# Performance work log

Hardware: AMD Instinct MI355X
Metric: run time of the kernel (lower is better)

## Reference

```python
import jax, jax.numpy as jnp
import numpy as np

B, L, D, H, DH, DL, NB = 8, 1024, 512, 8, 64, 64, 128
EPS = 1e-6


def layer_norm(x, g, b):
    m = jnp.mean(x, axis=-1, keepdims=True)
    v = jnp.mean((x - m) ** 2, axis=-1, keepdims=True)
    return (x - m) * jax.lax.rsqrt(v + EPS) * g + b


def rel_bias(timestamps, pos_w, ts_w):
    # position part: skew trick, pos_w has length 2L-1
    t = jnp.concatenate([pos_w, jnp.zeros((L,), pos_w.dtype)])  # (3L-1,)
    t = jnp.tile(t, L)[:-L].reshape(L, 3 * L - 2)
    rel_pos = t[:, L - 1:2 * L - 1]  # (L, L)
    # timestamp part: bucketized pairwise diffs of extended timestamps
    ext = jnp.concatenate([timestamps, timestamps[:, L - 1:L]], axis=1)  # (B, L+1)
    d = ext[:, 1:, None] - ext[:, None, :-1]  # (B, L, L)
    mag = jnp.maximum(jnp.abs(d).astype(jnp.float32), 1.0)
    bucket = jnp.clip((jnp.log(mag) / 0.301).astype(jnp.int32), 0, NB)
    rel_ts = ts_w[bucket]  # (B, L, L)
    return rel_pos[None] + rel_ts


def setup_inputs() -> dict:
    key = jax.random.key(0)
    ks = jax.random.split(key, 8)
    x = jax.random.normal(ks[0], (B, L, D), dtype=jnp.float32)
    timestamps = jnp.sort(jax.random.randint(ks[1], (B, L), 0, 1000000, dtype=jnp.int64), axis=1)
    attn_mask = jnp.triu(jnp.ones((L, L), jnp.float32), k=1)[None, None]  # 1 = masked (future)
    total_out = 2 * DL * H + 2 * DH * H
    uvqk_w = jax.random.normal(ks[2], (D, total_out), dtype=jnp.float32) * 0.02
    out_w = jax.random.normal(ks[3], (DL * H, D), dtype=jnp.float32) * 0.02
    out_b = jnp.zeros((D,), jnp.float32)
    ln1_g = jnp.ones((D,), jnp.float32); ln1_b = jnp.zeros((D,), jnp.float32)
    ln2_g = jnp.ones((DL * H,), jnp.float32); ln2_b = jnp.zeros((DL * H,), jnp.float32)
    ts_weights = jax.random.normal(ks[4], (NB + 1,), dtype=jnp.float32) * 0.02
    pos_weights = jax.random.normal(ks[5], (2 * L - 1,), dtype=jnp.float32) * 0.02
    return {"x": x, "timestamps": timestamps, "attn_mask": attn_mask,
            "uvqk_w": uvqk_w, "out_w": out_w, "out_b": out_b,
            "ln1_g": ln1_g, "ln1_b": ln1_b, "ln2_g": ln2_g, "ln2_b": ln2_b,
            "ts_weights": ts_weights, "pos_weights": pos_weights}


def reference(x, timestamps, attn_mask, uvqk_w, out_w, out_b,
              ln1_g, ln1_b, ln2_g, ln2_b, ts_weights, pos_weights):
    z = layer_norm(x, ln1_g, ln1_b)
    z = jax.nn.silu(z @ uvqk_w)  # linear_activation == 'silu'
    u, v, q, k = jnp.split(z, [DL * H, 2 * DL * H, 2 * DL * H + DH * H], axis=-1)
    q = q.reshape(B, L, H, DH)
    k = k.reshape(B, L, H, DH)
    v = v.reshape(B, L, H, DL)
    scores = jnp.einsum('bmhd,bnhd->bhmn', q, k)
    scores = scores + rel_bias(timestamps, pos_weights, ts_weights)[:, None]
    scores = jax.nn.silu(scores) / L * (1.0 - attn_mask)
    z = jnp.einsum('bhmn,bnhd->bmhd', scores, v).reshape(B, L, H * DL)
    z = layer_norm(z, ln2_g, ln2_b) * u  # gated LN
    return z @ out_w + out_b + x
```

## Files before the change

kernel.cpp:

```cpp
#include <hip/hip_runtime.h>
#include <math.h>

constexpr int Bc = 8;
constexpr int Lc = 1024;
constexpr int Dc = 512;
constexpr int Hc = 8;
constexpr int DHc = 64;
constexpr int DLc = 64;
constexpr int NBc = 128;
constexpr int TOTAL_OUT = 2 * DLc * Hc + 2 * DHc * Hc;
constexpr int ROWS = Bc * Lc;

using f32x4 = __attribute__((ext_vector_type(4))) float;
using s16x8 = __attribute__((ext_vector_type(8))) short;

__device__ __forceinline__ float bf2f(ushort u) {
    union { unsigned int i; float f; } v; v.i = ((unsigned int)u) << 16; return v.f;
}
__device__ __forceinline__ ushort f2bf(float f) {
    union { float f; unsigned int i; } v; v.f = f;
    unsigned int r = v.i + 0x7fffu + ((v.i >> 16) & 1u);
    return (ushort)(r >> 16);
}
__device__ __forceinline__ float silu(float x) {
    float e = __expf(-x);
    return x * __builtin_amdgcn_rcpf(1.0f + e);
}

__global__ __launch_bounds__(256) void transpose_cast(const float* __restrict__ in,
                                                      ushort* __restrict__ out,
                                                      int R, int C) {
    __shared__ float tile[32][33];
    int bc = blockIdx.x * 32, br = blockIdx.y * 32;
    int tx = threadIdx.x & 31, ty = threadIdx.x >> 5;
    for (int i = ty; i < 32; i += 8) {
        int r = br + i, c = bc + tx;
        tile[i][tx] = (r < R && c < C) ? in[(size_t)r * C + c] : 0.f;
    }
    __syncthreads();
    for (int i = ty; i < 32; i += 8) {
        int c = bc + i, r = br + tx;
        if (c < C && r < R) out[(size_t)c * R + r] = f2bf(tile[tx][i]);
    }
}

__global__ __launch_bounds__(256) void ln1_kernel(const float* __restrict__ x,
                                                  const float* __restrict__ g,
                                                  const float* __restrict__ bta,
                                                  ushort* __restrict__ outp) {
    int wid = threadIdx.x >> 6, lane = threadIdx.x & 63;
    int row = blockIdx.x * 4 + wid;
    const float4* xr = (const float4*)(x + (size_t)row * Dc);
    float4 a = xr[lane * 2], c = xr[lane * 2 + 1];
    float xv[8] = {a.x, a.y, a.z, a.w, c.x, c.y, c.z, c.w};
    float s = 0.f, q = 0.f;
#pragma unroll
    for (int i = 0; i < 8; i++) { s += xv[i]; q += xv[i] * xv[i]; }
#pragma unroll
    for (int off = 32; off; off >>= 1) { s += __shfl_xor(s, off); q += __shfl_xor(q, off); }
    float mean = s * (1.f / 512.f);
    float var  = q * (1.f / 512.f) - mean * mean;
    float rstd = rsqrtf(var + 1e-6f);
    const float4* gv = (const float4*)g; const float4* bv = (const float4*)bta;
    float4 g0 = gv[lane * 2], g1 = gv[lane * 2 + 1];
    float4 b0 = bv[lane * 2], b1 = bv[lane * 2 + 1];
    float G[8] = {g0.x, g0.y, g0.z, g0.w, g1.x, g1.y, g1.z, g1.w};
    float Bv[8] = {b0.x, b0.y, b0.z, b0.w, b1.x, b1.y, b1.z, b1.w};
    union { ushort u16[8]; uint4 v; } pk;
#pragma unroll
    for (int i = 0; i < 8; i++) pk.u16[i] = f2bf((xv[i] - mean) * rstd * G[i] + Bv[i]);
    ((uint4*)(outp + (size_t)row * Dc))[lane] = pk.v;
}

__global__ __launch_bounds__(256) void bias_kernel(const int* __restrict__ ts,
                                                   const float* __restrict__ pos_w,
                                                   const float* __restrict__ ts_w,
                                                   ushort* __restrict__ biasb) {
    __shared__ float posw[2 * Lc - 1];
    __shared__ float tsw[NBc + 1];
    int tid = threadIdx.x;
    int b = blockIdx.y;
    for (int i = tid; i < 2 * Lc - 1; i += 256) posw[i] = pos_w[i];
    if (tid < NBc + 1) tsw[tid] = ts_w[tid];
    __syncthreads();
    int m = blockIdx.x * 8 + (tid >> 5);
    int n0 = (tid & 31) * 32;
    const int* tsb = ts + b * Lc;
    int mp = m + 1 < Lc ? m + 1 : Lc - 1;
    int tsm = tsb[mp];
    int pbase = (Lc - 1) + n0 - m;
    union { ushort u16[32]; uint4 v[4]; } o;
#pragma unroll
    for (int i = 0; i < 32; i += 4) {
        int4 tn = *(const int4*)&tsb[n0 + i];
        int dv[4] = {tsm - tn.x, tsm - tn.y, tsm - tn.z, tsm - tn.w};
#pragma unroll
        for (int e = 0; e < 4; e++) {
            float mag = fmaxf(fabsf((float)dv[e]), 1.f);
            int bkt = (int)(__log2f(mag) * 2.3028147f);
            bkt = bkt < 0 ? 0 : (bkt > NBc ? NBc : bkt);
            o.u16[i + e] = f2bf(posw[pbase + i + e] + tsw[bkt]);
        }
    }
    uint4* dst = (uint4*)&biasb[((size_t)b * Lc + m) * Lc + n0];
#pragma unroll
    for (int i = 0; i < 4; i++) dst[i] = o.v[i];
}

__global__ __launch_bounds__(256) void gemm1_kernel(const ushort* __restrict__ A,
                                                    const ushort* __restrict__ Bt,
                                                    ushort* __restrict__ Ub,
                                                    ushort* __restrict__ VTg,
                                                    ushort* __restrict__ Qb,
                                                    ushort* __restrict__ Kb) {
    __shared__ __align__(16) ushort As[128][72];
    __shared__ __align__(16) ushort Bs[128][72];
    int tid = threadIdx.x;
    int m0 = blockIdx.x * 128, n0 = blockIdx.y * 128;
    int w = tid >> 6, lane = tid & 63;
    int wm = (w >> 1) * 64, wn = (w & 1) * 64;
    f32x4 acc[4][4] = {};
    for (int k0 = 0; k0 < Dc; k0 += 64) {
        __syncthreads();
#pragma unroll
        for (int c = tid; c < 1024; c += 256) {
            int r = c >> 3, c8 = c & 7;
            *(uint4*)&As[r][c8 * 8] = *(const uint4*)&A[(size_t)(m0 + r) * Dc + k0 + c8 * 8];
            *(uint4*)&Bs[r][c8 * 8] = *(const uint4*)&Bt[(size_t)(n0 + r) * Dc + k0 + c8 * 8];
        }
        __syncthreads();
#pragma unroll
        for (int ks = 0; ks < 2; ++ks) {
            int kb = ks * 32 + (lane >> 4) * 8;
            s16x8 af[4], bfr[4];
#pragma unroll
            for (int i = 0; i < 4; i++) af[i] = *(const s16x8*)&As[wm + i * 16 + (lane & 15)][kb];
#pragma unroll
            for (int j = 0; j < 4; j++) bfr[j] = *(const s16x8*)&Bs[wn + j * 16 + (lane & 15)][kb];
#pragma unroll
            for (int i = 0; i < 4; i++)
#pragma unroll
                for (int j = 0; j < 4; j++)
                    acc[i][j] = __builtin_amdgcn_mfma_f32_16x16x32_bf16(af[i], bfr[j], acc[i][j], 0, 0, 0);
        }
    }
    int lr = (lane >> 4) * 4, lc = lane & 15;
#pragma unroll
    for (int i = 0; i < 4; i++)
#pragma unroll
        for (int j = 0; j < 4; j++) {
            int col = n0 + wn + j * 16 + lc;
            int sect = col >> 9, cc = col & 511;
            int row0 = m0 + wm + i * 16 + lr;
            if (sect == 1) {
                int hh = cc >> 6, dd = cc & 63;
                int bb = row0 >> 10, nn = row0 & 1023;
                ushort4 pk;
                pk.x = f2bf(silu(acc[i][j][0]));
                pk.y = f2bf(silu(acc[i][j][1]));
                pk.z = f2bf(silu(acc[i][j][2]));
                pk.w = f2bf(silu(acc[i][j][3]));
                *(ushort4*)&VTg[((size_t)((bb * 8 + hh) * 64 + dd)) * 1024 + nn] = pk;
            } else {
                ushort* dst = (sect == 0) ? Ub : (sect == 2) ? Qb : Kb;
#pragma unroll
                for (int r = 0; r < 4; r++)
                    dst[(size_t)(row0 + r) * 512 + cc] = f2bf(silu(acc[i][j][r]));
            }
        }
}

__global__ __launch_bounds__(256) void attn_kernel(const ushort* __restrict__ Qb,
                                                   const ushort* __restrict__ Kb,
                                                   const ushort* __restrict__ VTg,
                                                   const ushort* __restrict__ biasb,
                                                   ushort* __restrict__ Ob) {
    int bx = blockIdx.x;
    int mt = (bx & 1) ? (bx >> 1) : (15 - (bx >> 1));
    int h = blockIdx.y, b = blockIdx.z;
    __shared__ __align__(16) ushort Ks[2][64][64];
    __shared__ __align__(16) ushort Ps[4][16][72];
    int tid = threadIdx.x, w = tid >> 6, lane = tid & 63;
    const size_t qkbase = ((size_t)b * Lc) * 512 + h * 64;
    const size_t vtbase = ((size_t)((b * 8 + h) * 64)) * 1024;
    const ushort* biasB = biasb + (size_t)b * Lc * Lc;
    const int m0 = mt * 64;
    int lc = lane & 15, g4 = lane >> 4, lr = g4 * 4;
    int sr = tid >> 2;
    int ss0 = (tid & 3) * 2;
    const ushort* kgrow = Kb + qkbase + (size_t)sr * 512;
    int dso0 = sr * 64 + (((ss0)     ^ (sr & 7)) * 8);
    int dso1 = sr * 64 + (((ss0 + 1) ^ (sr & 7)) * 8);

    {
        uint4 ka = *(const uint4*)(kgrow + ss0 * 8);
        uint4 kb_ = *(const uint4*)(kgrow + (ss0 + 1) * 8);
        *(uint4*)&(&Ks[0][0][0])[dso0] = ka;
        *(uint4*)&(&Ks[0][0][0])[dso1] = kb_;
    }
    __syncthreads();

    s16x8 qf[2];
#pragma unroll
    for (int ks = 0; ks < 2; ++ks)
        qf[ks] = *(const s16x8*)&Qb[qkbase + (size_t)(m0 + w * 16 + lc) * 512 + ks * 32 + g4 * 8];
    int mbase = m0 + w * 16 + lr;

    f32x4 acc_o[4] = {};
    int ntiles = mt + 1;
    int cur = 0;
    for (int nt = 0; nt < ntiles; ++nt) {
        int n0 = nt * 64;
        s16x8 vb[2][4];
#pragma unroll
        for (int ks = 0; ks < 2; ++ks)
#pragma unroll
            for (int j = 0; j < 4; j++)
                vb[ks][j] = *(const s16x8*)&VTg[vtbase + (size_t)(j * 16 + lc) * 1024 + n0 + ks * 32 + g4 * 8];
        ushort bsv[4][4];
#pragma unroll
        for (int j = 0; j < 4; j++)
#pragma unroll
            for (int r = 0; r < 4; r++)
                bsv[j][r] = biasB[(size_t)(mbase + r) * Lc + n0 + j * 16 + lc];
        bool hasnext = (nt + 1 < ntiles);
        uint4 ka = {}, kb_ = {};
        if (hasnext) {
            const ushort* kgn = kgrow + (size_t)(n0 + 64) * 512;
            ka  = *(const uint4*)(kgn + ss0 * 8);
            kb_ = *(const uint4*)(kgn + (ss0 + 1) * 8);
        }
        const ushort* ksb = &Ks[cur][0][0];
        f32x4 s[4] = {};
#pragma unroll
        for (int ks = 0; ks < 2; ++ks) {
            s16x8 kf[4];
#pragma unroll
            for (int j = 0; j < 4; j++)
                kf[j] = *(const s16x8*)&ksb[(j * 16 + lc) * 64 + (((ks * 4 + g4) ^ (lc & 7)) * 8)];
#pragma unroll
            for (int j = 0; j < 4; j++)
                s[j] = __builtin_amdgcn_mfma_f32_16x16x32_bf16(qf[ks], kf[j], s[j], 0, 0, 0);
        }
        bool diag = (nt == mt);
#pragma unroll
        for (int j = 0; j < 4; j++)
#pragma unroll
            for (int r = 0; r < 4; r++) {
                float sv = s[j][r] + bf2f(bsv[j][r]);
                float val = silu(sv) * (1.f / (float)Lc);
                if (diag && (j * 16 + lc) > (w * 16 + lr + r)) val = 0.f;
                Ps[w][lr + r][j * 16 + lc] = f2bf(val);
            }
#pragma unroll
        for (int ks = 0; ks < 2; ++ks) {
            s16x8 pa = *(const s16x8*)&Ps[w][lc][ks * 32 + g4 * 8];
#pragma unroll
            for (int j = 0; j < 4; j++)
                acc_o[j] = __builtin_amdgcn_mfma_f32_16x16x32_bf16(pa, vb[ks][j], acc_o[j], 0, 0, 0);
        }
        if (hasnext) {
            ushort* kd = &Ks[cur ^ 1][0][0];
            *(uint4*)&kd[dso0] = ka;
            *(uint4*)&kd[dso1] = kb_;
        }
        __syncthreads();
        cur ^= 1;
    }
#pragma unroll
    for (int j = 0; j < 4; j++)
#pragma unroll
        for (int r = 0; r < 4; r++) {
            int m = mbase + r;
            Ob[qkbase + (size_t)m * 512 + j * 16 + lc] = f2bf(acc_o[j][r]);
        }
}

__global__ __launch_bounds__(256) void ln2_kernel(const ushort* __restrict__ z,
                                                  const ushort* __restrict__ u,
                                                  const float* __restrict__ g,
                                                  const float* __restrict__ bta,
                                                  ushort* __restrict__ outp) {
    int wid = threadIdx.x >> 6, lane = threadIdx.x & 63;
    int row = blockIdx.x * 4 + wid;
    uint4 zv = ((const uint4*)(z + (size_t)row * 512))[lane];
    ushort* zu = (ushort*)&zv;
    float xv[8], s = 0.f, q = 0.f;
#pragma unroll
    for (int i = 0; i < 8; i++) { xv[i] = bf2f(zu[i]); s += xv[i]; q += xv[i] * xv[i]; }
#pragma unroll
    for (int off = 32; off; off >>= 1) { s += __shfl_xor(s, off); q += __shfl_xor(q, off); }
    float mean = s * (1.f / 512.f);
    float var  = q * (1.f / 512.f) - mean * mean;
    float rstd = rsqrtf(var + 1e-6f);
    uint4 uv = ((const uint4*)(u + (size_t)row * 512))[lane];
    ushort* uu = (ushort*)&uv;
    const float4* gv = (const float4*)g; const float4* bv = (const float4*)bta;
    float4 g0 = gv[lane * 2], g1 = gv[lane * 2 + 1];
    float4 b0 = bv[lane * 2], b1 = bv[lane * 2 + 1];
    float G[8] = {g0.x, g0.y, g0.z, g0.w, g1.x, g1.y, g1.z, g1.w};
    float Bv[8] = {b0.x, b0.y, b0.z, b0.w, b1.x, b1.y, b1.z, b1.w};
    union { ushort u16[8]; uint4 v; } pk;
#pragma unroll
    for (int i = 0; i < 8; i++)
        pk.u16[i] = f2bf(((xv[i] - mean) * rstd * G[i] + Bv[i]) * bf2f(uu[i]));
    ((uint4*)(outp + (size_t)row * 512))[lane] = pk.v;
}

__global__ __launch_bounds__(256) void gemm2_kernel(const ushort* __restrict__ A,
                                                    const ushort* __restrict__ Bt,
                                                    const float* __restrict__ ob,
                                                    const float* __restrict__ x,
                                                    float* __restrict__ outp) {
    __shared__ __align__(16) ushort As[128][72];
    __shared__ __align__(16) ushort Bs[128][72];
    int tid = threadIdx.x;
    int m0 = blockIdx.x * 128, n0 = blockIdx.y * 128;
    int w = tid >> 6, lane = tid & 63;
    int wm = (w >> 1) * 64, wn = (w & 1) * 64;
    f32x4 acc[4][4] = {};
    for (int k0 = 0; k0 < Dc; k0 += 64) {
        __syncthreads();
#pragma unroll
        for (int c = tid; c < 1024; c += 256) {
            int r = c >> 3, c8 = c & 7;
            *(uint4*)&As[r][c8 * 8] = *(const uint4*)&A[(size_t)(m0 + r) * Dc + k0 + c8 * 8];
            *(uint4*)&Bs[r][c8 * 8] = *(const uint4*)&Bt[(size_t)(n0 + r) * Dc + k0 + c8 * 8];
        }
        __syncthreads();
#pragma unroll
        for (int ks = 0; ks < 2; ++ks) {
            int kb = ks * 32 + (lane >> 4) * 8;
            s16x8 af[4], bfr[4];
#pragma unroll
            for (int i = 0; i < 4; i++) af[i] = *(const s16x8*)&As[wm + i * 16 + (lane & 15)][kb];
#pragma unroll
            for (int j = 0; j < 4; j++) bfr[j] = *(const s16x8*)&Bs[wn + j * 16 + (lane & 15)][kb];
#pragma unroll
            for (int i = 0; i < 4; i++)
#pragma unroll
                for (int j = 0; j < 4; j++)
                    acc[i][j] = __builtin_amdgcn_mfma_f32_16x16x32_bf16(af[i], bfr[j], acc[i][j], 0, 0, 0);
        }
    }
    int lr = (lane >> 4) * 4, lc = lane & 15;
#pragma unroll
    for (int i = 0; i < 4; i++)
#pragma unroll
        for (int j = 0; j < 4; j++) {
            int col = n0 + wn + j * 16 + lc;
            float bias = ob[col];
#pragma unroll
            for (int r = 0; r < 4; r++) {
                int row = m0 + wm + i * 16 + lr + r;
                size_t off = (size_t)row * 512 + col;
                outp[off] = acc[i][j][r] + bias + x[off];
            }
        }
}

extern "C" void kernel_launch(void* const* d_in, const int* in_sizes, int n_in,
                              void* d_out, int out_size, void* d_ws, size_t ws_size,
                              hipStream_t stream) {
    const float* x      = (const float*)d_in[0];
    const int*   tsp    = (const int*)d_in[1];
    const float* uvqk_w = (const float*)d_in[3];
    const float* out_w  = (const float*)d_in[4];
    const float* out_b  = (const float*)d_in[5];
    const float* ln1_g  = (const float*)d_in[6];
    const float* ln1_b  = (const float*)d_in[7];
    const float* ln2_g  = (const float*)d_in[8];
    const float* ln2_b  = (const float*)d_in[9];
    const float* ts_w   = (const float*)d_in[10];
    const float* pos_w  = (const float*)d_in[11];
    float* outp = (float*)d_out;

    char* ws = (char*)d_ws;
    size_t off = 0;
    auto alloc = [&](size_t bytes) { char* p = ws + off; off += (bytes + 255) & ~(size_t)255; return p; };
    const size_t MAT = (size_t)ROWS * 512 * sizeof(ushort);
    ushort* W1T = (ushort*)alloc((size_t)TOTAL_OUT * Dc * 2);
    ushort* W2T = (ushort*)alloc((size_t)Dc * Dc * 2);
    ushort* X1  = (ushort*)alloc(MAT);
    ushort* Ub  = (ushort*)alloc(MAT);
    ushort* VTg = (ushort*)alloc(MAT);
    ushort* Qb  = (ushort*)alloc(MAT);
    ushort* Kb  = (ushort*)alloc(MAT);
    ushort* Ob  = (ushort*)alloc(MAT);
    ushort* BIAS = (ushort*)alloc((size_t)Bc * Lc * Lc * 2);
    ushort* A2  = X1;

    transpose_cast<<<dim3(TOTAL_OUT / 32, Dc / 32), 256, 0, stream>>>(uvqk_w, W1T, Dc, TOTAL_OUT);
    transpose_cast<<<dim3(Dc / 32, Dc / 32), 256, 0, stream>>>(out_w, W2T, Dc, Dc);
    bias_kernel<<<dim3(Lc / 8, Bc), 256, 0, stream>>>(tsp, pos_w, ts_w, BIAS);
    ln1_kernel<<<ROWS / 4, 256, 0, stream>>>(x, ln1_g, ln1_b, X1);
    gemm1_kernel<<<dim3(ROWS / 128, TOTAL_OUT / 128), 256, 0, stream>>>(X1, W1T, Ub, VTg, Qb, Kb);
    attn_kernel<<<dim3(16, Hc, Bc), 256, 0, stream>>>(Qb, Kb, VTg, BIAS, Ob);
    ln2_kernel<<<ROWS / 4, 256, 0, stream>>>(Ob, Ub, ln2_g, ln2_b, A2);
    gemm2_kernel<<<dim3(ROWS / 128, Dc / 128), 256, 0, stream>>>(A2, W2T, out_b, x, outp);
}
```

Baseline: 274.7 us.

## Transpose score MFMA to get row-contiguous bias loads and packed P stores

Swaps the MFMA operand order for QK^T so each lane holds four consecutive key columns of one query row. This lets the bias be read as one 8-byte vector per tile instead of scattered 2-byte loads, and lets P be written with packed bf16 conversion into a swizzled unpadded LDS buffer. It also rotates the causal-tile index by batch to spread uneven work across blocks. The mask and the swizzle indexing must stay consistent with the PV read path.

```diff
diff --git a/kernel.cpp b/kernel.cpp
--- a/kernel.cpp
+++ b/kernel.cpp
@@ -21,6 +21,11 @@
     union { float f; unsigned int i; } v; v.f = f;
     unsigned int r = v.i + 0x7fffu + ((v.i >> 16) & 1u);
     return (ushort)(r >> 16);
+}
+__device__ __forceinline__ unsigned int cvtpk_bf16(float lo, float hi) {
+    unsigned int r;
+    asm("v_cvt_pk_bf16_f32 %0, %1, %2" : "=v"(r) : "v"(lo), "v"(hi));
+    return r;
 }
 __device__ __forceinline__ float silu(float x) {
     float e = __expf(-x);
@@ -176,16 +181,17 @@
                                                    const ushort* __restrict__ biasb,
                                                    ushort* __restrict__ Ob) {
     int bx = blockIdx.x;
-    int mt = (bx & 1) ? (bx >> 1) : (15 - (bx >> 1));
     int h = blockIdx.y, b = blockIdx.z;
+    int pidx = (bx + ((b >> 1) & 3)) & 15;
+    int mt = (pidx & 1) ? (pidx >> 1) : (15 - (pidx >> 1));
     __shared__ __align__(16) ushort Ks[2][64][64];
-    __shared__ __align__(16) ushort Ps[4][16][72];
+    __shared__ __align__(16) ushort Ps[4][16][64];
     int tid = threadIdx.x, w = tid >> 6, lane = tid & 63;
     const size_t qkbase = ((size_t)b * Lc) * 512 + h * 64;
     const size_t vtbase = ((size_t)((b * 8 + h) * 64)) * 1024;
     const ushort* biasB = biasb + (size_t)b * Lc * Lc;
     const int m0 = mt * 64;
-    int lc = lane & 15, g4 = lane >> 4, lr = g4 * 4;
+    int lc = lane & 15, g4 = lane >> 4;
     int sr = tid >> 2;
     int ss0 = (tid & 3) * 2;
     const ushort* kgrow = Kb + qkbase + (size_t)sr * 512;
@@ -200,12 +206,14 @@
     }
     __syncthreads();
 
+    const int mrow_in64 = w * 16 + lc;
+    const int mrow = m0 + mrow_in64;
     s16x8 qf[2];
 #pragma unroll
     for (int ks = 0; ks < 2; ++ks)
-        qf[ks] = *(const s16x8*)&Qb[qkbase + (size_t)(m0 + w * 16 + lc) * 512 + ks * 32 + g4 * 8];
-    int mbase = m0 + w * 16 + lr;
-
+        qf[ks] = *(const s16x8*)&Qb[qkbase + (size_t)mrow * 512 + ks * 32 + g4 * 8];
+
+    ushort* psW = &Ps[w][0][0];
     f32x4 acc_o[4] = {};
     int ntiles = mt + 1;
     int cur = 0;
@@ -217,12 +225,10 @@
 #pragma unroll
             for (int j = 0; j < 4; j++)
                 vb[ks][j] = *(const s16x8*)&VTg[vtbase + (size_t)(j * 16 + lc) * 1024 + n0 + ks * 32 + g4 * 8];
-        ushort bsv[4][4];
+        ushort4 bsv[4];
 #pragma unroll
         for (int j = 0; j < 4; j++)
-#pragma unroll
-            for (int r = 0; r < 4; r++)
-                bsv[j][r] = biasB[(size_t)(mbase + r) * Lc + n0 + j * 16 + lc];
+            bsv[j] = *(const ushort4*)&biasB[(size_t)mrow * Lc + n0 + j * 16 + g4 * 4];
         bool hasnext = (nt + 1 < ntiles);
         uint4 ka = {}, kb_ = {};
         if (hasnext) {
@@ -240,21 +246,31 @@
                 kf[j] = *(const s16x8*)&ksb[(j * 16 + lc) * 64 + (((ks * 4 + g4) ^ (lc & 7)) * 8)];
 #pragma unroll
             for (int j = 0; j < 4; j++)
-                s[j] = __builtin_amdgcn_mfma_f32_16x16x32_bf16(qf[ks], kf[j], s[j], 0, 0, 0);
+                s[j] = __builtin_amdgcn_mfma_f32_16x16x32_bf16(kf[j], qf[ks], s[j], 0, 0, 0);
         }
         bool diag = (nt == mt);
-#pragma unroll
-        for (int j = 0; j < 4; j++)
+        const ushort* bp;
+#pragma unroll
+        for (int j = 0; j < 4; j++) {
+            float p[4];
+            bp = (const ushort*)&bsv[j];
 #pragma unroll
             for (int r = 0; r < 4; r++) {
-                float sv = s[j][r] + bf2f(bsv[j][r]);
+                float sv = s[j][r] + bf2f(bp[r]);
                 float val = silu(sv) * (1.f / (float)Lc);
-                if (diag && (j * 16 + lc) > (w * 16 + lr + r)) val = 0.f;
-                Ps[w][lr + r][j * 16 + lc] = f2bf(val);
+                if (diag && (j * 16 + g4 * 4 + r) > mrow_in64) val = 0.f;
+                p[r] = val;
             }
+            unsigned int w0 = cvtpk_bf16(p[0], p[1]);
+            unsigned int w1 = cvtpk_bf16(p[2], p[3]);
+            int slot16 = j * 2 + (g4 >> 1);
+            int off = lc * 64 + ((slot16 ^ (lc & 7)) * 8) + (g4 & 1) * 4;
+            *(uint2*)&psW[off] = make_uint2(w0, w1);
+        }
 #pragma unroll
         for (int ks = 0; ks < 2; ++ks) {
-            s16x8 pa = *(const s16x8*)&Ps[w][lc][ks * 32 + g4 * 8];
+            int rs = ks * 4 + g4;
+            s16x8 pa = *(const s16x8*)&psW[lc * 64 + ((rs ^ (lc & 7)) * 8)];
 #pragma unroll
             for (int j = 0; j < 4; j++)
                 acc_o[j] = __builtin_amdgcn_mfma_f32_16x16x32_bf16(pa, vb[ks][j], acc_o[j], 0, 0, 0);
@@ -267,6 +283,7 @@
         __syncthreads();
         cur ^= 1;
     }
+    int mbase = m0 + w * 16 + g4 * 4;
 #pragma unroll
     for (int j = 0; j < 4; j++)
 #pragma unroll
```

Result: faster. 246.4 us (-10.3%).
